# Performance work log

Measured on AMD Instinct MI355X. Metric: run time of the kernel, lower is better.

Reference implementation:

```python
import jax, jax.numpy as jnp
import numpy as np

EMBED_DIM = 1024
NUM_HEADS = 16
HEAD_DIM = EMBED_DIM // NUM_HEADS  # 64
GROUP_SIZE = 4                     # 4 values packed per uint8 (2-bit KIVI)
Q_LEVELS = 3.0                     # 2-bit -> codes in [0, 3]
Q_HALF = 1.5                       # symmetric offset


def kivi_fake_quant(k):
    """Per-group 2-bit quantize+dequantize of keys, KIVI-style.
    k: [B, H, S, D] float32. Groups of GROUP_SIZE along D share one fp32 scale
    (mirrors k_cache_packed uint8 codes + k_scales fp32 in the source).
    """
    B, H, S, D = k.shape
    g = k.reshape(B, H, S, D // GROUP_SIZE, GROUP_SIZE)
    max_abs = jnp.max(jnp.abs(g), axis=-1, keepdims=True)        # per-group scale basis
    scale = max_abs / Q_HALF
    safe = jnp.where(scale == 0, 1.0, scale)
    codes = jnp.clip(jnp.round(g / safe + Q_HALF), 0.0, Q_LEVELS)  # uint8 codes (as float)
    deq = (codes - Q_HALF) * scale                                 # dequant
    return deq.reshape(B, H, S, D)


def split_heads(x):
    B, S, E = x.shape
    return x.reshape(B, S, NUM_HEADS, HEAD_DIM).transpose(0, 2, 1, 3)  # [B,H,S,d]


def setup_inputs() -> dict:
    key = jax.random.key(0)
    k1, k2, k3 = jax.random.split(key, 3)
    B, S = 4, 1024
    return {
        "hidden_states": jax.random.normal(k1, (B, S, EMBED_DIM), jnp.float32),
        "attention_mask": jnp.zeros((B, S), jnp.float32),  # additive mask
        "w_attn": jax.random.normal(k2, (EMBED_DIM, 3 * EMBED_DIM), jnp.float32) * 0.02,
        "b_attn": jnp.zeros((3 * EMBED_DIM,), jnp.float32),
        "w_proj": jax.random.normal(k3, (EMBED_DIM, EMBED_DIM), jnp.float32) * 0.02,
        "b_proj": jnp.zeros((EMBED_DIM,), jnp.float32),
    }


def reference(hidden_states, attention_mask, w_attn, b_attn, w_proj, b_proj):
    B, S, E = hidden_states.shape
    qkv = hidden_states @ w_attn + b_attn            # GPT-2 Conv1D: x @ W + b
    q, k, v = jnp.split(qkv, 3, axis=2)
    q, k, v = split_heads(q), split_heads(k), split_heads(v)   # [B,H,S,d]

    k_deq = kivi_fake_quant(k)                       # quantized KV cache (keys)
    # kivi_sycl.batched_attention: q @ dequant(K)^T over full cache_len (== S here)
    scores = jnp.einsum('bhqd,bhkd->bhqk', q, k_deq)
    # source adds 2-D additive mask BEFORE the 1/sqrt(d) scaling
    scores = scores + attention_mask[:, None, None, :]
    attn = jax.nn.softmax(scores / jnp.sqrt(jnp.float32(HEAD_DIM)), axis=-1)

    out = jnp.einsum('bhqk,bhkd->bhqd', attn, v)     # V cache kept fp32
    out = out.transpose(0, 2, 1, 3).reshape(B, S, E)
    return out @ w_proj + b_proj
```

## Files before the change

### kernel.cpp

```cpp
#include <hip/hip_runtime.h>
#include <math.h>

#define S_LEN 1024
#define B_SZ  4
#define E_DIM 1024
#define NH    16
#define HD    64
#define GK    1024

typedef unsigned short u16;
typedef _Float16 f16;
typedef __attribute__((ext_vector_type(8))) _Float16 f16x8;
typedef __attribute__((ext_vector_type(4))) float    f32x4;

#define MFMA16(a, b, c) __builtin_amdgcn_mfma_f32_16x16x32_f16(a, b, c, 0, 0, 0)
#define SCALE2 0.18033688011112042f

__device__ __forceinline__ u16 f2h_bits(float f) {
    union { f16 h; u16 u; } c; c.h = (f16)f;
    return c.u;
}
__device__ __forceinline__ unsigned pk2h(float a, float b) {
    return (unsigned)f2h_bits(a) | ((unsigned)f2h_bits(b) << 16);
}

__device__ __forceinline__ void glds16(const u16* g, u16* l) {
    __builtin_amdgcn_global_load_lds(
        (const __attribute__((address_space(1))) unsigned int*)g,
        (__attribute__((address_space(3))) unsigned int*)l, 16, 0, 0);
}

__global__ __launch_bounds__(256) void prep_all(
    const float* __restrict__ hs, u16* __restrict__ Hh,
    const float* __restrict__ w_attn, u16* __restrict__ Wqt,
    const float* __restrict__ w_proj, u16* __restrict__ Wpt)
{
    __shared__ float t[32][33];
    const int bid = blockIdx.x;

    if (bid < 4096) {
        const size_t i = ((size_t)bid * 256 + threadIdx.x) * 4;
        float4 v = *(const float4*)&hs[i];
        ushort4 h;
        h.x = f2h_bits(v.x); h.y = f2h_bits(v.y);
        h.z = f2h_bits(v.z); h.w = f2h_bits(v.w);
        *(ushort4*)&Hh[i] = h;
        return;
    }

    const bool isA = bid < 7168;
    const int tt = isA ? (bid - 4096) : (bid - 7168);
    const int bxx = isA ? (tt % 96) : (tt % 32);
    const int byy = isA ? (tt / 96) : (tt / 32);
    const int N   = isA ? 3072 : 1024;
    const float* W = isA ? w_attn : w_proj;
    u16* Wt = isA ? Wqt : Wpt;

    const int k0 = byy * 32, n0 = bxx * 32;
    {
        const int kr = threadIdx.x >> 3, nc = (threadIdx.x & 7) << 2;
        float4 v = *(const float4*)&W[(size_t)(k0 + kr) * N + n0 + nc];
        t[kr][nc] = v.x; t[kr][nc + 1] = v.y; t[kr][nc + 2] = v.z; t[kr][nc + 3] = v.w;
    }
    __syncthreads();
    const int nr = threadIdx.x >> 3, kc = (threadIdx.x & 7) << 2;
    ushort4 h;
    h.x = f2h_bits(t[kc + 0][nr]); h.y = f2h_bits(t[kc + 1][nr]);
    h.z = f2h_bits(t[kc + 2][nr]); h.w = f2h_bits(t[kc + 3][nr]);
    *(ushort4*)&Wt[(size_t)(n0 + nr) * GK + k0 + kc] = h;
}

__global__ __launch_bounds__(256, 3) void qkv_gemm(
    const u16* __restrict__ A, const u16* __restrict__ Bt,
    const float* __restrict__ bias, u16* __restrict__ Qh,
    u16* __restrict__ Kh, u16* __restrict__ Vtg)
{
    __shared__ u16 Asp[128 * 64];
    __shared__ u16 Bsp[128 * 64];

    const int tid = threadIdx.x;
    const int wave = tid >> 6, lane = tid & 63;
    const int quad = lane >> 4, l15 = lane & 15;
    const int wr = wave >> 1, wc = wave & 1;

    const int m0   = blockIdx.y * 128;
    const int nloc = blockIdx.x * 128;
    const int region = nloc >> 10;

    const u16* Ab = A  + (size_t)m0 * GK;
    const u16* Bb = Bt + (size_t)nloc * GK;

    const int soff = (((lane & 7) ^ ((lane >> 3) & 7)) << 3);
    const int srow8 = lane >> 3;
    const int sw = l15 & 7;

    f32x4 acc[4][4] = {};

    for (int k0 = 0; k0 < GK; k0 += 64) {
        __syncthreads();
        #pragma unroll
        for (int i = 0; i < 4; ++i) {
            const int tI = wave * 4 + i;
            const int row = tI * 8 + srow8;
            glds16(Ab + (size_t)row * GK + k0 + soff, &Asp[tI * 512]);
            glds16(Bb + (size_t)row * GK + k0 + soff, &Bsp[tI * 512]);
        }
        __syncthreads();
        #pragma unroll
        for (int h = 0; h < 2; ++h) {
            const int cs = ((4 * h + quad) ^ sw) << 3;
            f16x8 af[4], bf[4];
            #pragma unroll
            for (int i = 0; i < 4; ++i)
                af[i] = *(const f16x8*)&Asp[(64 * wr + 16 * i + l15) * 64 + cs];
            #pragma unroll
            for (int j = 0; j < 4; ++j)
                bf[j] = *(const f16x8*)&Bsp[(64 * wc + 16 * j + l15) * 64 + cs];
            #pragma unroll
            for (int i = 0; i < 4; ++i)
                #pragma unroll
                for (int j = 0; j < 4; ++j)
                    acc[i][j] = MFMA16(af[i], bf[j], acc[i][j]);
        }
    }

    #pragma unroll
    for (int j = 0; j < 4; ++j) {
        const int colg = nloc + 64 * wc + 16 * j + l15;
        const float bv = bias[colg];
        const int cr = colg & 1023, h = cr >> 6, d = cr & 63;
        #pragma unroll
        for (int i = 0; i < 4; ++i) {
            const int rowb = m0 + 64 * wr + 16 * i + quad * 4;
            const int b = rowb >> 10, s0 = rowb & 1023;
            if (region == 2) {
                float v0 = acc[i][j][0] + bv, v1 = acc[i][j][1] + bv;
                float v2 = acc[i][j][2] + bv, v3 = acc[i][j][3] + bv;
                uint2 st = { pk2h(v0, v1), pk2h(v2, v3) };
                *(uint2*)&Vtg[((size_t)(b * NH + h) * HD + d) * S_LEN + s0] = st;
            } else {
                #pragma unroll
                for (int r = 0; r < 4; ++r) {
                    float v = acc[i][j][r] + bv;
                    if (region == 1) {
                        float a = fabsf(v);
                        a = fmaxf(a, __shfl_xor(a, 1));
                        a = fmaxf(a, __shfl_xor(a, 2));
                        float scale = a * (1.0f / 1.5f);
                        float safe  = (scale == 0.0f) ? 1.0f : scale;
                        v = (fminf(fmaxf(rintf(v / safe + 1.5f), 0.0f), 3.0f) - 1.5f) * scale;
                    }
                    u16* dst = (region == 1) ? Kh : Qh;
                    dst[((size_t)(b * NH + h) * S_LEN + (s0 + r)) * HD + d] = f2h_bits(v);
                }
            }
        }
    }
}

__global__ __launch_bounds__(256, 4) void proj_gemm(
    const u16* __restrict__ A, const u16* __restrict__ Bt,
    const float* __restrict__ bias, float* __restrict__ C)
{
    __shared__ u16 Asp[64 * 64];
    __shared__ u16 Bsp[128 * 64];

    const int tid = threadIdx.x;
    const int wave = tid >> 6, lane = tid & 63;
    const int quad = lane >> 4, l15 = lane & 15;
    const int wr = wave >> 1, wc = wave & 1;

    const int m0   = blockIdx.y * 64;
    const int nloc = blockIdx.x * 128;

    const u16* Ab = A  + (size_t)m0 * GK;
    const u16* Bb = Bt + (size_t)nloc * GK;

    const int soff = (((lane & 7) ^ ((lane >> 3) & 7)) << 3);
    const int srow8 = lane >> 3;
    const int sw = l15 & 7;

    f32x4 acc[2][4] = {};

    for (int k0 = 0; k0 < GK; k0 += 64) {
        __syncthreads();
        #pragma unroll
        for (int i = 0; i < 2; ++i) {
            const int tI = wave * 2 + i;
            glds16(Ab + (size_t)(tI * 8 + srow8) * GK + k0 + soff, &Asp[tI * 512]);
        }
        #pragma unroll
        for (int i = 0; i < 4; ++i) {
            const int tI = wave * 4 + i;
            glds16(Bb + (size_t)(tI * 8 + srow8) * GK + k0 + soff, &Bsp[tI * 512]);
        }
        __syncthreads();
        #pragma unroll
        for (int h = 0; h < 2; ++h) {
            const int cs = ((4 * h + quad) ^ sw) << 3;
            f16x8 af[2], bf[4];
            #pragma unroll
            for (int i = 0; i < 2; ++i)
                af[i] = *(const f16x8*)&Asp[(32 * wr + 16 * i + l15) * 64 + cs];
            #pragma unroll
            for (int j = 0; j < 4; ++j)
                bf[j] = *(const f16x8*)&Bsp[(64 * wc + 16 * j + l15) * 64 + cs];
            #pragma unroll
            for (int i = 0; i < 2; ++i)
                #pragma unroll
                for (int j = 0; j < 4; ++j)
                    acc[i][j] = MFMA16(af[i], bf[j], acc[i][j]);
        }
    }

    #pragma unroll
    for (int j = 0; j < 4; ++j) {
        const int col = nloc + 64 * wc + 16 * j + l15;
        const float bv = bias[col];
        #pragma unroll
        for (int i = 0; i < 2; ++i) {
            const int row = m0 + 32 * wr + 16 * i + quad * 4;
            #pragma unroll
            for (int r = 0; r < 4; ++r)
                C[(size_t)(row + r) * E_DIM + col] = acc[i][j][r] + bv;
        }
    }
}

__global__ __launch_bounds__(256) void attn_mfma(
    const u16* __restrict__ Qh, const u16* __restrict__ Kh,
    const u16* __restrict__ Vtg, const float* __restrict__ mask,
    u16* __restrict__ out)
{
    __shared__ u16 KsL[64 * 64];
    __shared__ u16 VtL[64 * 64];
    __shared__ u16 Ps[4][16 * 72];

    const int tid  = threadIdx.x;
    const int wave = tid >> 6, lane = tid & 63;
    const int quad = lane >> 4, l15 = lane & 15;

    const int blk = blockIdx.x;
    const int qt = blk & 15;
    const int h  = (blk >> 4) & 15;
    const int b  = blk >> 8;
    const size_t head_base = (size_t)(b * NH + h) * (S_LEN * HD);

    const int qbase = qt * 64 + wave * 16;
    f16x8 qf0, qf1;
    {
        const u16* qp = Qh + head_base + (size_t)(qbase + l15) * HD + quad * 8;
        qf0 = *(const f16x8*)qp;
        qf1 = *(const f16x8*)(qp + 32);
    }

    f32x4 O[4] = {};
    float m_run = -INFINITY, l_run = 0.0f;

    const int srow_ = wave * 8 + (lane >> 3);
    const int skoff = (((lane & 7) ^ ((lane >> 3) & 7)) << 3);
    const int ch0 = (((0 + quad) ^ (l15 & 7)) << 3);
    const int ch1 = (((4 + quad) ^ (l15 & 7)) << 3);

    for (int kt = 0; kt < 16; ++kt) {
        __syncthreads();
        #pragma unroll
        for (int p = 0; p < 2; ++p) {
            const int srow = p * 32 + srow_;
            glds16(Kh  + head_base + (size_t)(kt * 64 + srow) * HD + skoff,
                   &KsL[p * 2048 + wave * 512]);
            glds16(Vtg + head_base + (size_t)srow * S_LEN + kt * 64 + skoff,
                   &VtL[p * 2048 + wave * 512]);
        }
        __syncthreads();

        f32x4 acc[4] = {};
        #pragma unroll
        for (int i = 0; i < 4; ++i) {
            const u16* kr = &KsL[(16 * i + l15) * 64];
            acc[i] = MFMA16(*(const f16x8*)&kr[ch0], qf0, acc[i]);
            acc[i] = MFMA16(*(const f16x8*)&kr[ch1], qf1, acc[i]);
        }

        const float* mrow = mask + b * S_LEN + kt * 64;
        float s[4][4];
        #pragma unroll
        for (int i = 0; i < 4; ++i) {
            float4 mk = *(const float4*)(mrow + 16 * i + quad * 4);
            s[i][0] = (acc[i][0] + mk.x) * SCALE2;
            s[i][1] = (acc[i][1] + mk.y) * SCALE2;
            s[i][2] = (acc[i][2] + mk.z) * SCALE2;
            s[i][3] = (acc[i][3] + mk.w) * SCALE2;
        }

        float tmax = s[0][0];
        #pragma unroll
        for (int i = 0; i < 4; ++i)
            #pragma unroll
            for (int r = 0; r < 4; ++r) tmax = fmaxf(tmax, s[i][r]);
        tmax = fmaxf(tmax, __shfl_xor(tmax, 16));
        tmax = fmaxf(tmax, __shfl_xor(tmax, 32));
        float mnew  = fmaxf(m_run, tmax);
        float alpha = exp2f(m_run - mnew);
        float p_[4][4], psum = 0.0f;
        #pragma unroll
        for (int i = 0; i < 4; ++i)
            #pragma unroll
            for (int r = 0; r < 4; ++r) { p_[i][r] = exp2f(s[i][r] - mnew); psum += p_[i][r]; }
        psum += __shfl_xor(psum, 16);
        psum += __shfl_xor(psum, 32);
        l_run = l_run * alpha + psum;
        m_run = mnew;

        {
            u16* pw = &Ps[wave][l15 * 72];
            #pragma unroll
            for (int i = 0; i < 4; ++i) {
                *(unsigned*)&pw[16 * i + quad * 4]     = pk2h(p_[i][0], p_[i][1]);
                *(unsigned*)&pw[16 * i + quad * 4 + 2] = pk2h(p_[i][2], p_[i][3]);
            }
        }

        float al[4];
        #pragma unroll
        for (int r = 0; r < 4; ++r) al[r] = __shfl(alpha, quad * 4 + r);
        #pragma unroll
        for (int i = 0; i < 4; ++i)
            #pragma unroll
            for (int r = 0; r < 4; ++r) O[i][r] *= al[r];

        #pragma unroll
        for (int kc = 0; kc < 2; ++kc) {
            f16x8 pa = *(const f16x8*)&Ps[wave][l15 * 72 + kc * 32 + quad * 8];
            const int chv = kc ? ch1 : ch0;
            #pragma unroll
            for (int i = 0; i < 4; ++i)
                O[i] = MFMA16(pa, *(const f16x8*)&VtL[(16 * i + l15) * 64 + chv], O[i]);
        }
    }

    float li[4];
    #pragma unroll
    for (int r = 0; r < 4; ++r) li[r] = 1.0f / __shfl(l_run, quad * 4 + r);
    #pragma unroll
    for (int r = 0; r < 4; ++r) {
        u16* orow = out + ((size_t)(b * S_LEN) + qbase + quad * 4 + r) * E_DIM
                    + h * HD + l15;
        orow[0]  = f2h_bits(O[0][r] * li[r]);
        orow[16] = f2h_bits(O[1][r] * li[r]);
        orow[32] = f2h_bits(O[2][r] * li[r]);
        orow[48] = f2h_bits(O[3][r] * li[r]);
    }
}

extern "C" void kernel_launch(void* const* d_in, const int* in_sizes, int n_in,
                              void* d_out, int out_size, void* d_ws, size_t ws_size,
                              hipStream_t stream)
{
    const float* hs     = (const float*)d_in[0];
    const float* mask   = (const float*)d_in[1];
    const float* w_attn = (const float*)d_in[2];
    const float* b_attn = (const float*)d_in[3];
    const float* w_proj = (const float*)d_in[4];
    const float* b_proj = (const float*)d_in[5];
    float* out = (float*)d_out;

    const size_t M1 = (size_t)4096 * 1024;
    u16* Ah   = (u16*)d_ws;
    u16* Wqt  = Ah   + M1;
    u16* Wpt  = Wqt  + 3 * M1;
    u16* Qh   = Wpt  + M1;
    u16* Kh   = Qh   + M1;
    u16* Vtg  = Kh   + M1;
    u16* AOh  = Vtg  + M1;

    prep_all<<<8192, 256, 0, stream>>>(hs, Ah, w_attn, Wqt, w_proj, Wpt);

    qkv_gemm<<<dim3(24, 32), 256, 0, stream>>>(Ah, Wqt, b_attn, Qh, Kh, Vtg);

    attn_mfma<<<B_SZ * NH * (S_LEN / 64), 256, 0, stream>>>(Qh, Kh, Vtg, mask, AOh);

    proj_gemm<<<dim3(8, 64), 256, 0, stream>>>(AOh, Wpt, b_proj, out);
}
```

Measured before the change: 191.9 us.

## Stage Q/K epilogue through LDS for coalesced stores; prescale mask, cheapen softmax

The QKV GEMM epilogue for the Q and K regions now writes the accumulators into shared memory, then reads whole rows back. This allows 16-byte coalesced global stores, and the KIVI group max is done in registers instead of with cross-lane shuffles. The mask is pre-multiplied by the softmax scale in an extra prep block, so the attention kernel folds it into one FMA per score. The softmax also uses the raw hardware exp2 and round-toward-zero packed fp16 conversion. The trade-offs are extra LDS traffic and two barriers in the GEMM epilogue, plus slightly different rounding of the P values.

Result: faster. 181.9 us (-5.2%).

```diff
diff --git a/kernel.cpp b/kernel.cpp
--- a/kernel.cpp
+++ b/kernel.cpp
@@ -11,6 +11,7 @@
 typedef unsigned short u16;
 typedef _Float16 f16;
 typedef __attribute__((ext_vector_type(8))) _Float16 f16x8;
+typedef __attribute__((ext_vector_type(2))) __fp16   hf16x2;
 typedef __attribute__((ext_vector_type(4))) float    f32x4;
 
 #define MFMA16(a, b, c) __builtin_amdgcn_mfma_f32_16x16x32_f16(a, b, c, 0, 0, 0)
@@ -22,6 +23,10 @@
 }
 __device__ __forceinline__ unsigned pk2h(float a, float b) {
     return (unsigned)f2h_bits(a) | ((unsigned)f2h_bits(b) << 16);
+}
+__device__ __forceinline__ unsigned pkrtz2(float a, float b) {
+    hf16x2 t = __builtin_amdgcn_cvt_pkrtz(a, b);
+    union { hf16x2 v; unsigned u; } c; c.v = t; return c.u;
 }
 
 __device__ __forceinline__ void glds16(const u16* g, u16* l) {
@@ -33,11 +38,22 @@
 __global__ __launch_bounds__(256) void prep_all(
     const float* __restrict__ hs, u16* __restrict__ Hh,
     const float* __restrict__ w_attn, u16* __restrict__ Wqt,
-    const float* __restrict__ w_proj, u16* __restrict__ Wpt)
+    const float* __restrict__ w_proj, u16* __restrict__ Wpt,
+    const float* __restrict__ mask, float* __restrict__ Msc)
 {
     __shared__ float t[32][33];
     const int bid = blockIdx.x;
 
+    if (bid == 8192) {
+        const int i = threadIdx.x * 16;
+        #pragma unroll
+        for (int k = 0; k < 4; ++k) {
+            float4 v = *(const float4*)&mask[i + 4 * k];
+            float4 o = { v.x * SCALE2, v.y * SCALE2, v.z * SCALE2, v.w * SCALE2 };
+            *(float4*)&Msc[i + 4 * k] = o;
+        }
+        return;
+    }
     if (bid < 4096) {
         const size_t i = ((size_t)bid * 256 + threadIdx.x) * 4;
         float4 v = *(const float4*)&hs[i];
@@ -75,8 +91,9 @@
     const float* __restrict__ bias, u16* __restrict__ Qh,
     u16* __restrict__ Kh, u16* __restrict__ Vtg)
 {
-    __shared__ u16 Asp[128 * 64];
-    __shared__ u16 Bsp[128 * 64];
+    __shared__ u16 SLDS[16896];
+    u16* Asp = SLDS;
+    u16* Bsp = SLDS + 8192;
 
     const int tid = threadIdx.x;
     const int wave = tid >> 6, lane = tid & 63;
@@ -124,35 +141,75 @@
         }
     }
 
-    #pragma unroll
-    for (int j = 0; j < 4; ++j) {
-        const int colg = nloc + 64 * wc + 16 * j + l15;
-        const float bv = bias[colg];
-        const int cr = colg & 1023, h = cr >> 6, d = cr & 63;
-        #pragma unroll
-        for (int i = 0; i < 4; ++i) {
-            const int rowb = m0 + 64 * wr + 16 * i + quad * 4;
-            const int b = rowb >> 10, s0 = rowb & 1023;
-            if (region == 2) {
+    if (region == 2) {
+        #pragma unroll
+        for (int j = 0; j < 4; ++j) {
+            const int colg = nloc + 64 * wc + 16 * j + l15;
+            const float bv = bias[colg];
+            const int cr = colg & 1023, h = cr >> 6, d = cr & 63;
+            #pragma unroll
+            for (int i = 0; i < 4; ++i) {
+                const int rowb = m0 + 64 * wr + 16 * i + quad * 4;
+                const int b = rowb >> 10, s0 = rowb & 1023;
                 float v0 = acc[i][j][0] + bv, v1 = acc[i][j][1] + bv;
                 float v2 = acc[i][j][2] + bv, v3 = acc[i][j][3] + bv;
                 uint2 st = { pk2h(v0, v1), pk2h(v2, v3) };
                 *(uint2*)&Vtg[((size_t)(b * NH + h) * HD + d) * S_LEN + s0] = st;
-            } else {
+            }
+        }
+    } else {
+        float* EP = (float*)SLDS;
+        u16* dstg = (region == 1) ? Kh : Qh;
+        #pragma unroll
+        for (int p = 0; p < 2; ++p) {
+            __syncthreads();
+            if (wr == p) {
                 #pragma unroll
-                for (int r = 0; r < 4; ++r) {
-                    float v = acc[i][j][r] + bv;
-                    if (region == 1) {
-                        float a = fabsf(v);
-                        a = fmaxf(a, __shfl_xor(a, 1));
-                        a = fmaxf(a, __shfl_xor(a, 2));
-                        float scale = a * (1.0f / 1.5f);
-                        float safe  = (scale == 0.0f) ? 1.0f : scale;
-                        v = (fminf(fmaxf(rintf(v / safe + 1.5f), 0.0f), 3.0f) - 1.5f) * scale;
+                for (int i = 0; i < 4; ++i)
+                    #pragma unroll
+                    for (int j = 0; j < 4; ++j) {
+                        const int colb = 64 * wc + 16 * j + l15;
+                        const float bv = bias[nloc + colb];
+                        #pragma unroll
+                        for (int r = 0; r < 4; ++r)
+                            EP[(16 * i + quad * 4 + r) * 132 + colb] = acc[i][j][r] + bv;
                     }
-                    u16* dst = (region == 1) ? Kh : Qh;
-                    dst[((size_t)(b * NH + h) * S_LEN + (s0 + r)) * HD + d] = f2h_bits(v);
+            }
+            __syncthreads();
+            const int rr = tid >> 2, cc = (tid & 3) * 32;
+            const int rowg = m0 + 64 * p + rr;
+            const int bb = rowg >> 10, ss = rowg & 1023;
+            float v[32];
+            #pragma unroll
+            for (int k = 0; k < 8; ++k) {
+                f32x4 t4 = *(const f32x4*)&EP[rr * 132 + cc + 4 * k];
+                v[4 * k + 0] = t4[0]; v[4 * k + 1] = t4[1];
+                v[4 * k + 2] = t4[2]; v[4 * k + 3] = t4[3];
+            }
+            if (region == 1) {
+                #pragma unroll
+                for (int g = 0; g < 8; ++g) {
+                    float a = fmaxf(fmaxf(fabsf(v[4 * g]), fabsf(v[4 * g + 1])),
+                                    fmaxf(fabsf(v[4 * g + 2]), fabsf(v[4 * g + 3])));
+                    float scale = a * (1.0f / 1.5f);
+                    float safe  = (scale == 0.0f) ? 1.0f : scale;
+                    #pragma unroll
+                    for (int r = 0; r < 4; ++r) {
+                        float q = fminf(fmaxf(rintf(v[4 * g + r] / safe + 1.5f), 0.0f), 3.0f);
+                        v[4 * g + r] = (q - 1.5f) * scale;
+                    }
                 }
+            }
+            unsigned w[16];
+            #pragma unroll
+            for (int m = 0; m < 16; ++m) w[m] = pk2h(v[2 * m], v[2 * m + 1]);
+            const int hh = ((nloc & 1023) + cc) >> 6;
+            const int d0 = cc & 63;
+            u16* dp = dstg + (((size_t)(bb * NH + hh)) * S_LEN + ss) * HD + d0;
+            #pragma unroll
+            for (int q4 = 0; q4 < 4; ++q4) {
+                uint4 st = { w[4 * q4], w[4 * q4 + 1], w[4 * q4 + 2], w[4 * q4 + 3] };
+                *(uint4*)&dp[q4 * 8] = st;
             }
         }
     }
@@ -229,7 +286,7 @@
 
 __global__ __launch_bounds__(256) void attn_mfma(
     const u16* __restrict__ Qh, const u16* __restrict__ Kh,
-    const u16* __restrict__ Vtg, const float* __restrict__ mask,
+    const u16* __restrict__ Vtg, const float* __restrict__ Msc,
     u16* __restrict__ out)
 {
     __shared__ u16 KsL[64 * 64];
@@ -282,31 +339,36 @@
             acc[i] = MFMA16(*(const f16x8*)&kr[ch1], qf1, acc[i]);
         }
 
-        const float* mrow = mask + b * S_LEN + kt * 64;
-        float s[4][4];
+        const float* mrow = Msc + b * S_LEN + kt * 64;
+        f32x4 s4[4];
         #pragma unroll
         for (int i = 0; i < 4; ++i) {
-            float4 mk = *(const float4*)(mrow + 16 * i + quad * 4);
-            s[i][0] = (acc[i][0] + mk.x) * SCALE2;
-            s[i][1] = (acc[i][1] + mk.y) * SCALE2;
-            s[i][2] = (acc[i][2] + mk.z) * SCALE2;
-            s[i][3] = (acc[i][3] + mk.w) * SCALE2;
-        }
-
-        float tmax = s[0][0];
-        #pragma unroll
-        for (int i = 0; i < 4; ++i)
-            #pragma unroll
-            for (int r = 0; r < 4; ++r) tmax = fmaxf(tmax, s[i][r]);
+            f32x4 mk = *(const f32x4*)(mrow + 16 * i + quad * 4);
+            s4[i] = acc[i] * SCALE2 + mk;
+        }
+
+        float t0 = fmaxf(fmaxf(fmaxf(s4[0][0], s4[0][1]), s4[0][2]), s4[0][3]);
+        float t1 = fmaxf(fmaxf(fmaxf(s4[1][0], s4[1][1]), s4[1][2]), s4[1][3]);
+        float t2 = fmaxf(fmaxf(fmaxf(s4[2][0], s4[2][1]), s4[2][2]), s4[2][3]);
+        float t3 = fmaxf(fmaxf(fmaxf(s4[3][0], s4[3][1]), s4[3][2]), s4[3][3]);
+        float tmax = fmaxf(fmaxf(t0, t1), fmaxf(t2, t3));
         tmax = fmaxf(tmax, __shfl_xor(tmax, 16));
         tmax = fmaxf(tmax, __shfl_xor(tmax, 32));
         float mnew  = fmaxf(m_run, tmax);
-        float alpha = exp2f(m_run - mnew);
-        float p_[4][4], psum = 0.0f;
-        #pragma unroll
-        for (int i = 0; i < 4; ++i)
-            #pragma unroll
-            for (int r = 0; r < 4; ++r) { p_[i][r] = exp2f(s[i][r] - mnew); psum += p_[i][r]; }
+        float alpha = __builtin_amdgcn_exp2f(m_run - mnew);
+
+        f32x4 p4[4];
+        f32x4 ps4 = {0.f, 0.f, 0.f, 0.f};
+        #pragma unroll
+        for (int i = 0; i < 4; ++i) {
+            f32x4 d = s4[i] - mnew;
+            p4[i][0] = __builtin_amdgcn_exp2f(d[0]);
+            p4[i][1] = __builtin_amdgcn_exp2f(d[1]);
+            p4[i][2] = __builtin_amdgcn_exp2f(d[2]);
+            p4[i][3] = __builtin_amdgcn_exp2f(d[3]);
+            ps4 += p4[i];
+        }
+        float psum = (ps4[0] + ps4[1]) + (ps4[2] + ps4[3]);
         psum += __shfl_xor(psum, 16);
         psum += __shfl_xor(psum, 32);
         l_run = l_run * alpha + psum;
@@ -316,18 +378,18 @@
             u16* pw = &Ps[wave][l15 * 72];
             #pragma unroll
             for (int i = 0; i < 4; ++i) {
-                *(unsigned*)&pw[16 * i + quad * 4]     = pk2h(p_[i][0], p_[i][1]);
-                *(unsigned*)&pw[16 * i + quad * 4 + 2] = pk2h(p_[i][2], p_[i][3]);
-            }
-        }
-
-        float al[4];
-        #pragma unroll
-        for (int r = 0; r < 4; ++r) al[r] = __shfl(alpha, quad * 4 + r);
-        #pragma unroll
-        for (int i = 0; i < 4; ++i)
-            #pragma unroll
-            for (int r = 0; r < 4; ++r) O[i][r] *= al[r];
+                *(unsigned*)&pw[16 * i + quad * 4]     = pkrtz2(p4[i][0], p4[i][1]);
+                *(unsigned*)&pw[16 * i + quad * 4 + 2] = pkrtz2(p4[i][2], p4[i][3]);
+            }
+        }
+
+        f32x4 al4;
+        al4[0] = __shfl(alpha, quad * 4 + 0);
+        al4[1] = __shfl(alpha, quad * 4 + 1);
+        al4[2] = __shfl(alpha, quad * 4 + 2);
+        al4[3] = __shfl(alpha, quad * 4 + 3);
+        #pragma unroll
+        for (int i = 0; i < 4; ++i) O[i] *= al4;
 
         #pragma unroll
         for (int kc = 0; kc < 2; ++kc) {
@@ -373,12 +435,13 @@
     u16* Kh   = Qh   + M1;
     u16* Vtg  = Kh   + M1;
     u16* AOh  = Vtg  + M1;
-
-    prep_all<<<8192, 256, 0, stream>>>(hs, Ah, w_attn, Wqt, w_proj, Wpt);
+    float* Msc = (float*)(AOh + M1);
+
+    prep_all<<<8193, 256, 0, stream>>>(hs, Ah, w_attn, Wqt, w_proj, Wpt, mask, Msc);
 
     qkv_gemm<<<dim3(24, 32), 256, 0, stream>>>(Ah, Wqt, b_attn, Qh, Kh, Vtg);
 
-    attn_mfma<<<B_SZ * NH * (S_LEN / 64), 256, 0, stream>>>(Qh, Kh, Vtg, mask, AOh);
+    attn_mfma<<<B_SZ * NH * (S_LEN / 64), 256, 0, stream>>>(Qh, Kh, Vtg, Msc, AOh);
 
     proj_gemm<<<dim3(8, 64), 256, 0, stream>>>(AOh, Wpt, b_proj, out);
 }
```
